# Kernel tuning notes

Measured on AMD Instinct MI355X. Metric: run time of the kernel, lower is better.

The kernel has to match this reference:

```python
import jax, jax.numpy as jnp
import numpy as np

BS, L, D = 32, 512, 512
N_CHARS = 32
DICT = 97

def setup_inputs() -> dict:
    key = jax.random.key(0)
    ks = jax.random.split(key, 10)
    s = 1.0 / np.sqrt(D)
    return {
        "inp": jax.random.normal(ks[0], (BS, L, D), jnp.float32),
        "emb": jax.random.normal(ks[1], (N_CHARS, D), jnp.float32) * 0.02,  # embedding table; char_orders == arange
        "Wo_w": jax.random.normal(ks[2], (D, D), jnp.float32) * s,
        "Wo_b": jnp.zeros((D,), jnp.float32),
        "Wv_w": jax.random.normal(ks[3], (D, D), jnp.float32) * s,
        "Wv_b": jnp.zeros((D,), jnp.float32),
        "We_w": jax.random.normal(ks[4], (D, 1), jnp.float32) * s,
        "We_b": jnp.zeros((1,), jnp.float32),
        "Wc_w": jax.random.normal(ks[5], (D, DICT), jnp.float32) * s,
        "Wc_b": jnp.zeros((DICT,), jnp.float32),
    }

def reference(inp, emb, Wo_w, Wo_b, Wv_w, Wv_b, We_w, We_b, Wc_w, Wc_b):
    # O = embedding(arange(max_n_chars)) is just the full embedding table: (n, d)
    w_o = emb @ Wo_w + Wo_b                      # (n, d)
    w_v = inp @ Wv_w + Wv_b                      # (b, L, d)
    # broadcast add -> tanh -> score projection: (b, n, L, d) -> (b, n, L)
    h = jnp.tanh(w_o[None, :, None, :] + w_v[:, None, :, :])
    e = jnp.einsum('bnld,d->bnl', h, We_w[:, 0]) + We_b[0]
    alpha = jax.nn.softmax(e, axis=2)            # softmax over L (axis=2)
    visual_features = jnp.einsum('bnl,bld->bnd', alpha, inp)  # (b, n, d)
    logits = visual_features @ Wc_w + Wc_b       # (b, n, dict)
    return (visual_features, logits)
```

## Files before the change

kernel.cpp:

```cpp
#include <hip/hip_runtime.h>
#include <hip/hip_bf16.h>

#define BS    32
#define LSEQ  512
#define DIM   512
#define NCH   32
#define NDICT 97
#define CHB   16

#define TANH_SCALE 2.8853900817779268f

typedef __attribute__((ext_vector_type(8))) short bf16x8;
typedef __attribute__((ext_vector_type(4))) float f32x4;

#define GLDS16(gsrc, ldst) \
  __builtin_amdgcn_global_load_lds((const __attribute__((address_space(1))) void*)(gsrc), \
                                   (__attribute__((address_space(3))) void*)(ldst), 16, 0, 0)

__device__ __forceinline__ float sig_from_scaled(float xs) {
    float e2 = __builtin_amdgcn_exp2f(xs);
    return __builtin_amdgcn_rcpf(1.0f + e2);
}

__device__ __forceinline__ void split_bf16(float a, ushort& h, ushort& l) {
    __hip_bfloat16 bh = __float2bfloat16(a);
    float fh = __bfloat162float(bh);
    __hip_bfloat16 bl = __float2bfloat16(a - fh);
    h = *(ushort*)&bh; l = *(ushort*)&bl;
}

__global__ __launch_bounds__(256) void k_prep_a(
    const float* __restrict__ in, ushort* __restrict__ hiT, ushort* __restrict__ loT)
{
    __shared__ float tile[64][65];
    const int bid = blockIdx.x;
    const int b  = bid >> 6;
    const int l0 = ((bid >> 3) & 7) * 64;
    const int d0 = (bid & 7) * 64;
    const int t  = threadIdx.x;
    const int tr = t >> 4, tc = (t & 15) * 4;

    #pragma unroll
    for (int rr = 0; rr < 4; ++rr) {
        const int l = l0 + rr * 16 + tr;
        float4 v = *(const float4*)&in[((size_t)(b * LSEQ) + l) * DIM + d0 + tc];
        tile[rr * 16 + tr][tc + 0] = v.x; tile[rr * 16 + tr][tc + 1] = v.y;
        tile[rr * 16 + tr][tc + 2] = v.z; tile[rr * 16 + tr][tc + 3] = v.w;
    }
    __syncthreads();
    #pragma unroll
    for (int rr = 0; rr < 4; ++rr) {
        const int dd = rr * 16 + tr;
        ushort4 h, l4;
        split_bf16(tile[tc + 0][dd], h.x, l4.x);
        split_bf16(tile[tc + 1][dd], h.y, l4.y);
        split_bf16(tile[tc + 2][dd], h.z, l4.z);
        split_bf16(tile[tc + 3][dd], h.w, l4.w);
        const size_t o = ((size_t)(b * DIM) + d0 + dd) * LSEQ + l0 + tc;
        *(ushort4*)&hiT[o] = h;
        *(ushort4*)&loT[o] = l4;
    }
}

__global__ __launch_bounds__(256) void k_misc(
    const float* __restrict__ Wv, ushort* __restrict__ BhiT, ushort* __restrict__ BloT,
    const float* __restrict__ emb, const float* __restrict__ Wo_w,
    const float* __restrict__ Wo_b, float* __restrict__ w_o)
{
    __shared__ float tile[64][65];
    const int bid = blockIdx.x;
    const int t = threadIdx.x;
    if (bid < 64) {
        const int k0 = (bid >> 3) * 64, n0 = (bid & 7) * 64;
        const int tr = t >> 4, tc = (t & 15) * 4;
        #pragma unroll
        for (int rr = 0; rr < 64; rr += 16) {
            float4 v = *(const float4*)&Wv[(k0 + rr + tr) * DIM + n0 + tc];
            tile[rr + tr][tc + 0] = v.x; tile[rr + tr][tc + 1] = v.y;
            tile[rr + tr][tc + 2] = v.z; tile[rr + tr][tc + 3] = v.w;
        }
        __syncthreads();
        #pragma unroll
        for (int rr = 0; rr < 64; rr += 16) {
            const int n = rr + tr;
            ushort4 h, l;
            split_bf16(tile[tc + 0][n], h.x, l.x);
            split_bf16(tile[tc + 1][n], h.y, l.y);
            split_bf16(tile[tc + 2][n], h.z, l.z);
            split_bf16(tile[tc + 3][n], h.w, l.w);
            *(ushort4*)&BhiT[(size_t)(n0 + n) * DIM + k0 + tc] = h;
            *(ushort4*)&BloT[(size_t)(n0 + n) * DIM + k0 + tc] = l;
        }
    } else {
        const int n = bid - 64;
        float* embS = &tile[0][0];
        embS[t]       = emb[n * DIM + t];
        embS[t + 256] = emb[n * DIM + t + 256];
        __syncthreads();
        float acc0 = Wo_b[t], acc1 = Wo_b[t + 256];
        for (int k = 0; k < DIM; ++k) {
            float ek = embS[k];
            acc0 = fmaf(ek, Wo_w[k * DIM + t], acc0);
            acc1 = fmaf(ek, Wo_w[k * DIM + t + 256], acc1);
        }
        w_o[n * DIM + t]       = acc0 * TANH_SCALE;
        w_o[n * DIM + t + 256] = acc1 * TANH_SCALE;
    }
}

__global__ __launch_bounds__(256) void k_gemm(
    const float* __restrict__ A,
    const ushort* __restrict__ Bhi, const ushort* __restrict__ Blo,
    const float* __restrict__ bias, float* __restrict__ C)
{
    __shared__ ushort Bh[128 * 64], Bl[128 * 64];

    const int bid = blockIdx.x;
    const int mb = (bid & 7) * 16 + (bid >> 5);
    const int nb = (bid >> 3) & 3;
    const int bm = mb * 128, bn = nb * 128;

    const int t = threadIdx.x;
    const int wave = t >> 6, lane = t & 63;
    const int wm = wave >> 1, wn = wave & 1;

    const int rl = lane >> 3;
    const int gsw = (lane & 7) ^ rl;

    const int am = bm + wm * 64 + (lane & 15);
    const int ak = (lane >> 4) * 8;

    f32x4 acc[4][4] = {};

    for (int k0 = 0; k0 < DIM; k0 += 64) {
        bf16x8 ah[4][2], al[4][2];
        #pragma unroll
        for (int i = 0; i < 4; ++i)
            #pragma unroll
            for (int kh = 0; kh < 2; ++kh) {
                const float* ap = A + (size_t)(am + i * 16) * DIM + k0 + kh * 32 + ak;
                float4 v0 = *(const float4*)ap;
                float4 v1 = *(const float4*)(ap + 4);
                float vv[8] = {v0.x, v0.y, v0.z, v0.w, v1.x, v1.y, v1.z, v1.w};
                bf16x8 h, l;
                #pragma unroll
                for (int q = 0; q < 8; ++q) {
                    ushort hq, lq; split_bf16(vv[q], hq, lq);
                    h[q] = (short)hq; l[q] = (short)lq;
                }
                ah[i][kh] = h; al[i][kh] = l;
            }
        #pragma unroll
        for (int c4 = 0; c4 < 4; ++c4) {
            const int c = wave * 4 + c4;
            const size_t rb = (size_t)(bn + c * 8 + rl) * DIM + k0 + gsw * 8;
            GLDS16(Bhi + rb, &Bh[c * 512]);
            GLDS16(Blo + rb, &Bl[c * 512]);
        }
        __syncthreads();

        #pragma unroll
        for (int kh = 0; kh < 2; ++kh) {
            const int p = ((kh * 4 + (lane >> 4)) ^ (lane & 7)) * 8;
            bf16x8 bh[4], bl[4];
            #pragma unroll
            for (int j = 0; j < 4; ++j) {
                const int rbr = (wn * 64 + j * 16 + (lane & 15)) * 64 + p;
                bh[j] = *(const bf16x8*)&Bh[rbr];
                bl[j] = *(const bf16x8*)&Bl[rbr];
            }
            #pragma unroll
            for (int i = 0; i < 4; ++i)
                #pragma unroll
                for (int j = 0; j < 4; ++j) {
                    acc[i][j] = __builtin_amdgcn_mfma_f32_16x16x32_bf16(ah[i][kh], bh[j], acc[i][j], 0, 0, 0);
                    acc[i][j] = __builtin_amdgcn_mfma_f32_16x16x32_bf16(ah[i][kh], bl[j], acc[i][j], 0, 0, 0);
                    acc[i][j] = __builtin_amdgcn_mfma_f32_16x16x32_bf16(al[i][kh], bh[j], acc[i][j], 0, 0, 0);
                }
        }
        __syncthreads();
    }

    #pragma unroll
    for (int i = 0; i < 4; ++i) {
        const int m = bm + wm * 64 + i * 16 + (lane >> 4) * 4;
        #pragma unroll
        for (int j = 0; j < 4; ++j) {
            const int n = bn + wn * 64 + j * 16 + (lane & 15);
            const float bb = bias[n];
            #pragma unroll
            for (int r = 0; r < 4; ++r)
                C[(size_t)(m + r) * DIM + n] = acc[i][j][r] + bb;
        }
    }
}

__global__ __launch_bounds__(256, 4) void k_e(
    const float* __restrict__ w_v, const float* __restrict__ w_o,
    const float* __restrict__ We_w, float* __restrict__ e)
{
    __shared__ float4 woS[CHB * 128];
    const int lblk = blockIdx.x;
    const int b    = blockIdx.y;
    const int ch0  = blockIdx.z * CHB;
    const int t    = threadIdx.x;

    const float4* wog = ((const float4*)w_o) + ch0 * (DIM / 4);
    #pragma unroll
    for (int i = 0; i < 8; ++i)
        woS[t + 256 * i] = wog[t + 256 * i];

    const int wave = t >> 6, lane = t & 63;
    const int g = lane >> 4, j = lane & 15;
    const int l = lblk * 16 + wave * 4 + g;

    const float4* wvp = (const float4*)(w_v + (size_t)(b * LSEQ + l) * DIM);
    const float4* wep = (const float4*)We_w;
    float4 wv[8], we[8];
    #pragma unroll
    for (int k = 0; k < 8; ++k) {
        wv[k] = wvp[16 * k + j];
        we[k] = wep[16 * k + j];
    }
    #pragma unroll
    for (int k = 0; k < 8; ++k) {
        wv[k].x *= TANH_SCALE; wv[k].y *= TANH_SCALE;
        wv[k].z *= TANH_SCALE; wv[k].w *= TANH_SCALE;
    }
    float wsum = 0.0f;
    #pragma unroll
    for (int k = 0; k < 8; ++k)
        wsum += (we[k].x + we[k].y) + (we[k].z + we[k].w);
    #pragma unroll
    for (int off = 1; off < 16; off <<= 1) wsum += __shfl_xor(wsum, off, 64);

    __syncthreads();

    float res = 0.0f;
    for (int i = 0; i < CHB; ++i) {
        const float4* wrow = &woS[i * 128];
        float s = 0.0f;
        #pragma unroll
        for (int k = 0; k < 8; ++k) {
            float4 wo4 = wrow[16 * k + j];
            s = fmaf(we[k].x, sig_from_scaled(wo4.x + wv[k].x), s);
            s = fmaf(we[k].y, sig_from_scaled(wo4.y + wv[k].y), s);
            s = fmaf(we[k].z, sig_from_scaled(wo4.z + wv[k].z), s);
            s = fmaf(we[k].w, sig_from_scaled(wo4.w + wv[k].w), s);
        }
        #pragma unroll
        for (int off = 1; off < 16; off <<= 1) s += __shfl_xor(s, off, 64);
        if (j == i) res = s;
    }
    e[(size_t)(b * NCH + ch0 + j) * LSEQ + l] = fmaf(-2.0f, res, wsum);
}

__global__ __launch_bounds__(256) void k_soft(
    const float* __restrict__ e, ushort* __restrict__ aH, ushort* __restrict__ aL)
{
    const int row = blockIdx.x * 4 + (threadIdx.x >> 6);
    const int lane = threadIdx.x & 63;
    const float4* erow = (const float4*)(e + (size_t)row * LSEQ);
    float4 v0 = erow[2 * lane], v1 = erow[2 * lane + 1];
    float m = fmaxf(fmaxf(fmaxf(v0.x, v0.y), fmaxf(v0.z, v0.w)),
                    fmaxf(fmaxf(v1.x, v1.y), fmaxf(v1.z, v1.w)));
    #pragma unroll
    for (int off = 32; off > 0; off >>= 1) m = fmaxf(m, __shfl_xor(m, off, 64));
    float p[8];
    p[0] = __expf(v0.x - m); p[1] = __expf(v0.y - m);
    p[2] = __expf(v0.z - m); p[3] = __expf(v0.w - m);
    p[4] = __expf(v1.x - m); p[5] = __expf(v1.y - m);
    p[6] = __expf(v1.z - m); p[7] = __expf(v1.w - m);
    float s = ((p[0] + p[1]) + (p[2] + p[3])) + ((p[4] + p[5]) + (p[6] + p[7]));
    #pragma unroll
    for (int off = 32; off > 0; off >>= 1) s += __shfl_xor(s, off, 64);
    const float inv = 1.0f / s;
    ushort4 h0, h1, l0, l1;
    split_bf16(p[0] * inv, h0.x, l0.x); split_bf16(p[1] * inv, h0.y, l0.y);
    split_bf16(p[2] * inv, h0.z, l0.z); split_bf16(p[3] * inv, h0.w, l0.w);
    split_bf16(p[4] * inv, h1.x, l1.x); split_bf16(p[5] * inv, h1.y, l1.y);
    split_bf16(p[6] * inv, h1.z, l1.z); split_bf16(p[7] * inv, h1.w, l1.w);
    ushort4* oh = (ushort4*)(aH + (size_t)row * LSEQ);
    ushort4* ol = (ushort4*)(aL + (size_t)row * LSEQ);
    oh[2 * lane] = h0; oh[2 * lane + 1] = h1;
    ol[2 * lane] = l0; ol[2 * lane + 1] = l1;
}

__global__ __launch_bounds__(256) void k_vf(
    const ushort* __restrict__ AhiT, const ushort* __restrict__ AloT,
    const ushort* __restrict__ aH, const ushort* __restrict__ aL,
    float* __restrict__ out_vf)
{
    __shared__ ushort BsH[NCH * LSEQ / 1];
    __shared__ ushort BsL[NCH * LSEQ / 1];
    const int dg = blockIdx.x, b = blockIdx.y;
    const int t = threadIdx.x;
    const int wave = t >> 6, lane = t & 63;

    const ushort* baseH = aH + (size_t)(b * NCH) * LSEQ;
    const ushort* baseL = aL + (size_t)(b * NCH) * LSEQ;
    #pragma unroll
    for (int q = 0; q < 16; ++q) {
        const int idx = wave * 16 + q;
        const int p = idx & 1, n = idx >> 1;
        const int gsrc = lane ^ (n & 7);
        const ushort* src = (p ? baseL : baseH) + (size_t)n * LSEQ + gsrc * 8;
        ushort* dst = (p ? BsL : BsH) + n * LSEQ;
        GLDS16(src, dst);
    }
    __syncthreads();

    const int d = dg * 64 + wave * 16 + (lane & 15);
    const ushort* arow_h = AhiT + ((size_t)(b * DIM) + d) * LSEQ;
    const ushort* arow_l = AloT + ((size_t)(b * DIM) + d) * LSEQ;
    const int koff = (lane >> 4) * 8;

    f32x4 acc[2] = {};
    #pragma unroll 4
    for (int s = 0; s < 16; ++s) {
        bf16x8 ah = *(const bf16x8*)&arow_h[s * 32 + koff];
        bf16x8 al = *(const bf16x8*)&arow_l[s * 32 + koff];
        const int g = ((s * 4 + (lane >> 4)) ^ (lane & 7)) * 8;
        #pragma unroll
        for (int j = 0; j < 2; ++j) {
            const int n = j * 16 + (lane & 15);
            bf16x8 bh = *(const bf16x8*)&BsH[n * LSEQ + g];
            bf16x8 bl = *(const bf16x8*)&BsL[n * LSEQ + g];
            acc[j] = __builtin_amdgcn_mfma_f32_16x16x32_bf16(ah, bh, acc[j], 0, 0, 0);
            acc[j] = __builtin_amdgcn_mfma_f32_16x16x32_bf16(ah, bl, acc[j], 0, 0, 0);
            acc[j] = __builtin_amdgcn_mfma_f32_16x16x32_bf16(al, bh, acc[j], 0, 0, 0);
        }
    }

    const int dw = dg * 64 + wave * 16 + (lane >> 4) * 4;
    #pragma unroll
    for (int j = 0; j < 2; ++j) {
        const int n = j * 16 + (lane & 15);
        #pragma unroll
        for (int r = 0; r < 4; ++r)
            out_vf[(size_t)(b * NCH + n) * DIM + dw + r] = acc[j][r];
    }
}

__global__ __launch_bounds__(256) void k_lg(
    const float* __restrict__ vf, const float* __restrict__ Wc_w,
    const float* __restrict__ Wc_b, float* __restrict__ out_logits)
{
    __shared__ float vfS[DIM];
    __shared__ float lgS[2][NDICT];
    const int row = blockIdx.x;
    const int t = threadIdx.x;
    const float2 v2 = ((const float2*)(vf + (size_t)row * DIM))[t];
    vfS[2 * t] = v2.x; vfS[2 * t + 1] = v2.y;
    __syncthreads();
    const int j = t & 127, half = t >> 7;
    if (j < NDICT) {
        const float* wc = Wc_w + half * 256 * NDICT + j;
        const float* vv = &vfS[half * 256];
        float a = 0.0f;
        #pragma unroll 4
        for (int d = 0; d < 256; ++d)
            a = fmaf(vv[d], wc[d * NDICT], a);
        lgS[half][j] = a;
    }
    __syncthreads();
    if (t < NDICT)
        out_logits[(size_t)row * NDICT + t] = Wc_b[t] + lgS[0][t] + lgS[1][t];
}

extern "C" void kernel_launch(void* const* d_in, const int* in_sizes, int n_in,
                              void* d_out, int out_size, void* d_ws, size_t ws_size,
                              hipStream_t stream)
{
    const float* inp  = (const float*)d_in[0];
    const float* emb  = (const float*)d_in[1];
    const float* Wo_w = (const float*)d_in[2];
    const float* Wo_b = (const float*)d_in[3];
    const float* Wv_w = (const float*)d_in[4];
    const float* Wv_b = (const float*)d_in[5];
    const float* We_w = (const float*)d_in[6];
    const float* Wc_w = (const float*)d_in[8];
    const float* Wc_b = (const float*)d_in[9];

    char* p = (char*)d_ws;
    float*  w_o  = (float*)p;   p += (64 << 10);
    float*  ev   = (float*)p;   p += (size_t)BS * NCH * LSEQ * 4;
    ushort* BhiT = (ushort*)p;  p += (size_t)DIM * DIM * 2;
    ushort* BloT = (ushort*)p;  p += (size_t)DIM * DIM * 2;
    ushort* aH   = (ushort*)p;  p += (size_t)BS * NCH * LSEQ * 2;
    ushort* aL   = (ushort*)p;  p += (size_t)BS * NCH * LSEQ * 2;
    ushort* AhiT = (ushort*)p;  p += (size_t)BS * LSEQ * DIM * 2;
    ushort* AloT = (ushort*)p;  p += (size_t)BS * LSEQ * DIM * 2;
    float*  w_v  = (float*)p;

    float* out_vf = (float*)d_out;
    float* out_lg = out_vf + BS * NCH * DIM;

    k_prep_a<<<dim3(2048), dim3(256), 0, stream>>>(inp, AhiT, AloT);
    k_misc<<<dim3(96), dim3(256), 0, stream>>>(Wv_w, BhiT, BloT, emb, Wo_w, Wo_b, w_o);
    k_gemm<<<dim3(512), dim3(256), 0, stream>>>(inp, BhiT, BloT, Wv_b, w_v);
    k_e<<<dim3(LSEQ / 16, BS, NCH / CHB), dim3(256), 0, stream>>>(w_v, w_o, We_w, ev);
    k_soft<<<dim3(256), dim3(256), 0, stream>>>(ev, aH, aL);
    k_vf<<<dim3(8, BS), dim3(256), 0, stream>>>(AhiT, AloT, aH, aL, (float*)d_out);
    k_lg<<<dim3(BS * NCH), dim3(256), 0, stream>>>((const float*)d_out, Wc_w, Wc_b, out_lg);
}
```

Measured before the change: 174.6 us.

## Fuse input transpose/split into k_vf, fold tanh scale into Wv, batch logits rows

The separate k_prep_a pass, which transposed the input and split it into bf16 hi/lo arrays in global memory, is removed. k_vf now loads fp32 input tiles itself, splits them into a swizzled LDS layout, and runs the MFMA with the roles of the A and B operands swapped. The tanh scale is folded into the Wv hi/lo weights and the bias at prep time instead of being applied in k_e. k_lg now handles four rows per block so each Wc_w load is reused across four rows. Together this drops a full round trip through global memory of the input, at the cost of extra LDS work and barriers inside k_vf.

```diff
diff --git a/kernel.cpp b/kernel.cpp
--- a/kernel.cpp
+++ b/kernel.cpp
@@ -29,39 +29,6 @@
     h = *(ushort*)&bh; l = *(ushort*)&bl;
 }
 
-__global__ __launch_bounds__(256) void k_prep_a(
-    const float* __restrict__ in, ushort* __restrict__ hiT, ushort* __restrict__ loT)
-{
-    __shared__ float tile[64][65];
-    const int bid = blockIdx.x;
-    const int b  = bid >> 6;
-    const int l0 = ((bid >> 3) & 7) * 64;
-    const int d0 = (bid & 7) * 64;
-    const int t  = threadIdx.x;
-    const int tr = t >> 4, tc = (t & 15) * 4;
-
-    #pragma unroll
-    for (int rr = 0; rr < 4; ++rr) {
-        const int l = l0 + rr * 16 + tr;
-        float4 v = *(const float4*)&in[((size_t)(b * LSEQ) + l) * DIM + d0 + tc];
-        tile[rr * 16 + tr][tc + 0] = v.x; tile[rr * 16 + tr][tc + 1] = v.y;
-        tile[rr * 16 + tr][tc + 2] = v.z; tile[rr * 16 + tr][tc + 3] = v.w;
-    }
-    __syncthreads();
-    #pragma unroll
-    for (int rr = 0; rr < 4; ++rr) {
-        const int dd = rr * 16 + tr;
-        ushort4 h, l4;
-        split_bf16(tile[tc + 0][dd], h.x, l4.x);
-        split_bf16(tile[tc + 1][dd], h.y, l4.y);
-        split_bf16(tile[tc + 2][dd], h.z, l4.z);
-        split_bf16(tile[tc + 3][dd], h.w, l4.w);
-        const size_t o = ((size_t)(b * DIM) + d0 + dd) * LSEQ + l0 + tc;
-        *(ushort4*)&hiT[o] = h;
-        *(ushort4*)&loT[o] = l4;
-    }
-}
-
 __global__ __launch_bounds__(256) void k_misc(
     const float* __restrict__ Wv, ushort* __restrict__ BhiT, ushort* __restrict__ BloT,
     const float* __restrict__ emb, const float* __restrict__ Wo_w,
@@ -84,10 +51,10 @@
         for (int rr = 0; rr < 64; rr += 16) {
             const int n = rr + tr;
             ushort4 h, l;
-            split_bf16(tile[tc + 0][n], h.x, l.x);
-            split_bf16(tile[tc + 1][n], h.y, l.y);
-            split_bf16(tile[tc + 2][n], h.z, l.z);
-            split_bf16(tile[tc + 3][n], h.w, l.w);
+            split_bf16(tile[tc + 0][n] * TANH_SCALE, h.x, l.x);
+            split_bf16(tile[tc + 1][n] * TANH_SCALE, h.y, l.y);
+            split_bf16(tile[tc + 2][n] * TANH_SCALE, h.z, l.z);
+            split_bf16(tile[tc + 3][n] * TANH_SCALE, h.w, l.w);
             *(ushort4*)&BhiT[(size_t)(n0 + n) * DIM + k0 + tc] = h;
             *(ushort4*)&BloT[(size_t)(n0 + n) * DIM + k0 + tc] = l;
         }
@@ -187,7 +154,7 @@
         #pragma unroll
         for (int j = 0; j < 4; ++j) {
             const int n = bn + wn * 64 + j * 16 + (lane & 15);
-            const float bb = bias[n];
+            const float bb = TANH_SCALE * bias[n];
             #pragma unroll
             for (int r = 0; r < 4; ++r)
                 C[(size_t)(m + r) * DIM + n] = acc[i][j][r] + bb;
@@ -221,11 +188,6 @@
     for (int k = 0; k < 8; ++k) {
         wv[k] = wvp[16 * k + j];
         we[k] = wep[16 * k + j];
-    }
-    #pragma unroll
-    for (int k = 0; k < 8; ++k) {
-        wv[k].x *= TANH_SCALE; wv[k].y *= TANH_SCALE;
-        wv[k].z *= TANH_SCALE; wv[k].w *= TANH_SCALE;
     }
     float wsum = 0.0f;
     #pragma unroll
@@ -287,58 +249,78 @@
 }
 
 __global__ __launch_bounds__(256) void k_vf(
-    const ushort* __restrict__ AhiT, const ushort* __restrict__ AloT,
+    const float* __restrict__ inp,
     const ushort* __restrict__ aH, const ushort* __restrict__ aL,
     float* __restrict__ out_vf)
 {
-    __shared__ ushort BsH[NCH * LSEQ / 1];
-    __shared__ ushort BsL[NCH * LSEQ / 1];
+    __shared__ unsigned int tT[64 * 68];
     const int dg = blockIdx.x, b = blockIdx.y;
     const int t = threadIdx.x;
     const int wave = t >> 6, lane = t & 63;
-
-    const ushort* baseH = aH + (size_t)(b * NCH) * LSEQ;
-    const ushort* baseL = aL + (size_t)(b * NCH) * LSEQ;
-    #pragma unroll
-    for (int q = 0; q < 16; ++q) {
-        const int idx = wave * 16 + q;
-        const int p = idx & 1, n = idx >> 1;
-        const int gsrc = lane ^ (n & 7);
-        const ushort* src = (p ? baseL : baseH) + (size_t)n * LSEQ + gsrc * 8;
-        ushort* dst = (p ? BsL : BsH) + n * LSEQ;
-        GLDS16(src, dst);
-    }
-    __syncthreads();
-
-    const int d = dg * 64 + wave * 16 + (lane & 15);
-    const ushort* arow_h = AhiT + ((size_t)(b * DIM) + d) * LSEQ;
-    const ushort* arow_l = AloT + ((size_t)(b * DIM) + d) * LSEQ;
-    const int koff = (lane >> 4) * 8;
+    const int d0 = dg * 64;
+    const int lr = t >> 2;
+    const int dcb = (t & 3) * 4;
+
+    const ushort* aHb = aH + (size_t)b * NCH * LSEQ + (size_t)(lane & 15) * LSEQ;
+    const ushort* aLb = aL + (size_t)b * NCH * LSEQ + (size_t)(lane & 15) * LSEQ;
+    const int dl = wave * 16 + (lane & 15);
+    const int lloc = (lane >> 4) * 8;
 
     f32x4 acc[2] = {};
-    #pragma unroll 4
-    for (int s = 0; s < 16; ++s) {
-        bf16x8 ah = *(const bf16x8*)&arow_h[s * 32 + koff];
-        bf16x8 al = *(const bf16x8*)&arow_l[s * 32 + koff];
-        const int g = ((s * 4 + (lane >> 4)) ^ (lane & 7)) * 8;
-        #pragma unroll
-        for (int j = 0; j < 2; ++j) {
-            const int n = j * 16 + (lane & 15);
-            bf16x8 bh = *(const bf16x8*)&BsH[n * LSEQ + g];
-            bf16x8 bl = *(const bf16x8*)&BsL[n * LSEQ + g];
-            acc[j] = __builtin_amdgcn_mfma_f32_16x16x32_bf16(ah, bh, acc[j], 0, 0, 0);
-            acc[j] = __builtin_amdgcn_mfma_f32_16x16x32_bf16(ah, bl, acc[j], 0, 0, 0);
-            acc[j] = __builtin_amdgcn_mfma_f32_16x16x32_bf16(al, bh, acc[j], 0, 0, 0);
-        }
-    }
-
-    const int dw = dg * 64 + wave * 16 + (lane >> 4) * 4;
-    #pragma unroll
-    for (int j = 0; j < 2; ++j) {
-        const int n = j * 16 + (lane & 15);
+
+    for (int l0 = 0; l0 < LSEQ; l0 += 64) {
+        #pragma unroll
+        for (int q = 0; q < 4; ++q) {
+            const int dc = dcb + 16 * q;
+            float4 v = *(const float4*)&inp[((size_t)(b * LSEQ) + l0 + lr) * DIM + d0 + dc];
+            float vv[4] = {v.x, v.y, v.z, v.w};
+            #pragma unroll
+            for (int i = 0; i < 4; ++i) {
+                ushort h, l; split_bf16(vv[i], h, l);
+                const int d = dc + i;
+                const int g = (lr >> 3) ^ (d & 7);
+                tT[d * 68 + g * 8 + (lr & 7)] = ((unsigned)l << 16) | (unsigned)h;
+            }
+        }
+        __syncthreads();
+        #pragma unroll
+        for (int sl = 0; sl < 2; ++sl) {
+            const int ll = sl * 32 + lloc;
+            const int gg = ((ll >> 3) ^ (dl & 7)) * 8;
+            const uint4* srcp = (const uint4*)&tT[dl * 68 + gg];
+            uint4 w0 = srcp[0], w1 = srcp[1];
+            union { unsigned u[4]; bf16x8 v; } H, L;
+            H.u[0] = (w0.x & 0xFFFFu) | (w0.y << 16);
+            H.u[1] = (w0.z & 0xFFFFu) | (w0.w << 16);
+            H.u[2] = (w1.x & 0xFFFFu) | (w1.y << 16);
+            H.u[3] = (w1.z & 0xFFFFu) | (w1.w << 16);
+            L.u[0] = (w0.x >> 16) | (w0.y & 0xFFFF0000u);
+            L.u[1] = (w0.z >> 16) | (w0.w & 0xFFFF0000u);
+            L.u[2] = (w1.x >> 16) | (w1.y & 0xFFFF0000u);
+            L.u[3] = (w1.z >> 16) | (w1.w & 0xFFFF0000u);
+
+            const bf16x8 ah0 = *(const bf16x8*)&aHb[l0 + ll];
+            const bf16x8 ah1 = *(const bf16x8*)&aHb[16 * LSEQ + l0 + ll];
+            const bf16x8 al0 = *(const bf16x8*)&aLb[l0 + ll];
+            const bf16x8 al1 = *(const bf16x8*)&aLb[16 * LSEQ + l0 + ll];
+
+            acc[0] = __builtin_amdgcn_mfma_f32_16x16x32_bf16(ah0, H.v, acc[0], 0, 0, 0);
+            acc[0] = __builtin_amdgcn_mfma_f32_16x16x32_bf16(ah0, L.v, acc[0], 0, 0, 0);
+            acc[0] = __builtin_amdgcn_mfma_f32_16x16x32_bf16(al0, H.v, acc[0], 0, 0, 0);
+            acc[1] = __builtin_amdgcn_mfma_f32_16x16x32_bf16(ah1, H.v, acc[1], 0, 0, 0);
+            acc[1] = __builtin_amdgcn_mfma_f32_16x16x32_bf16(ah1, L.v, acc[1], 0, 0, 0);
+            acc[1] = __builtin_amdgcn_mfma_f32_16x16x32_bf16(al1, H.v, acc[1], 0, 0, 0);
+        }
+        __syncthreads();
+    }
+
+    const int dcol = d0 + dl;
+    #pragma unroll
+    for (int m = 0; m < 2; ++m) {
+        const int ch = m * 16 + (lane >> 4) * 4;
         #pragma unroll
         for (int r = 0; r < 4; ++r)
-            out_vf[(size_t)(b * NCH + n) * DIM + dw + r] = acc[j][r];
+            out_vf[(size_t)(b * NCH + ch + r) * DIM + dcol] = acc[m][r];
     }
 }
 
@@ -346,26 +328,40 @@
     const float* __restrict__ vf, const float* __restrict__ Wc_w,
     const float* __restrict__ Wc_b, float* __restrict__ out_logits)
 {
-    __shared__ float vfS[DIM];
-    __shared__ float lgS[2][NDICT];
-    const int row = blockIdx.x;
+    __shared__ float vfS[4][DIM];
+    __shared__ float lgS[2][4][NDICT];
+    const int r0 = blockIdx.x * 4;
     const int t = threadIdx.x;
-    const float2 v2 = ((const float2*)(vf + (size_t)row * DIM))[t];
-    vfS[2 * t] = v2.x; vfS[2 * t + 1] = v2.y;
+    const int wave = t >> 6, lane = t & 63;
+
+    const float2* src = (const float2*)(vf + (size_t)(r0 + wave) * DIM);
+    #pragma unroll
+    for (int q = 0; q < 4; ++q)
+        ((float2*)&vfS[wave][0])[lane + 64 * q] = src[lane + 64 * q];
     __syncthreads();
+
     const int j = t & 127, half = t >> 7;
     if (j < NDICT) {
-        const float* wc = Wc_w + half * 256 * NDICT + j;
-        const float* vv = &vfS[half * 256];
-        float a = 0.0f;
+        const float* wc = Wc_w + (size_t)half * 256 * NDICT + j;
+        const float* v0 = &vfS[0][half * 256];
+        const float* v1 = &vfS[1][half * 256];
+        const float* v2 = &vfS[2][half * 256];
+        const float* v3 = &vfS[3][half * 256];
+        float a0 = 0.f, a1 = 0.f, a2 = 0.f, a3 = 0.f;
         #pragma unroll 4
-        for (int d = 0; d < 256; ++d)
-            a = fmaf(vv[d], wc[d * NDICT], a);
-        lgS[half][j] = a;
+        for (int d = 0; d < 256; ++d) {
+            float w = wc[(size_t)d * NDICT];
+            a0 = fmaf(v0[d], w, a0); a1 = fmaf(v1[d], w, a1);
+            a2 = fmaf(v2[d], w, a2); a3 = fmaf(v3[d], w, a3);
+        }
+        lgS[half][0][j] = a0; lgS[half][1][j] = a1;
+        lgS[half][2][j] = a2; lgS[half][3][j] = a3;
     }
     __syncthreads();
-    if (t < NDICT)
-        out_logits[(size_t)row * NDICT + t] = Wc_b[t] + lgS[0][t] + lgS[1][t];
+    for (int idx = t; idx < 4 * NDICT; idx += 256) {
+        const int r = idx / NDICT, jj = idx - r * NDICT;
+        out_logits[(size_t)(r0 + r) * NDICT + jj] = Wc_b[jj] + lgS[0][r][jj] + lgS[1][r][jj];
+    }
 }
 
 extern "C" void kernel_launch(void* const* d_in, const int* in_sizes, int n_in,
@@ -389,18 +385,15 @@
     ushort* BloT = (ushort*)p;  p += (size_t)DIM * DIM * 2;
     ushort* aH   = (ushort*)p;  p += (size_t)BS * NCH * LSEQ * 2;
     ushort* aL   = (ushort*)p;  p += (size_t)BS * NCH * LSEQ * 2;
-    ushort* AhiT = (ushort*)p;  p += (size_t)BS * LSEQ * DIM * 2;
-    ushort* AloT = (ushort*)p;  p += (size_t)BS * LSEQ * DIM * 2;
     float*  w_v  = (float*)p;
 
     float* out_vf = (float*)d_out;
     float* out_lg = out_vf + BS * NCH * DIM;
 
-    k_prep_a<<<dim3(2048), dim3(256), 0, stream>>>(inp, AhiT, AloT);
     k_misc<<<dim3(96), dim3(256), 0, stream>>>(Wv_w, BhiT, BloT, emb, Wo_w, Wo_b, w_o);
     k_gemm<<<dim3(512), dim3(256), 0, stream>>>(inp, BhiT, BloT, Wv_b, w_v);
     k_e<<<dim3(LSEQ / 16, BS, NCH / CHB), dim3(256), 0, stream>>>(w_v, w_o, We_w, ev);
     k_soft<<<dim3(256), dim3(256), 0, stream>>>(ev, aH, aL);
-    k_vf<<<dim3(8, BS), dim3(256), 0, stream>>>(AhiT, AloT, aH, aL, (float*)d_out);
-    k_lg<<<dim3(BS * NCH), dim3(256), 0, stream>>>((const float*)d_out, Wc_w, Wc_b, out_lg);
-}
+    k_vf<<<dim3(8, BS), dim3(256), 0, stream>>>(inp, aH, aL, out_vf);
+    k_lg<<<dim3(256), dim3(256), 0, stream>>>(out_vf, Wc_w, Wc_b, out_lg);
+}
```

Measured after the change: 170.8 us. 2.2% less time.
